# Kernel optimization log

Measured on AMD Instinct MI355X. Metric: run time of the kernel, lower is better.

The kernel has to match this reference:

```python
import jax, jax.numpy as jnp
import numpy as np

B = 16384   # batch of nodes
K = 15      # num_sample neighbors (default in forward)
U = 19997   # unique neighbor ids (prime so stride trick gives distinct ids)
D = 256     # feature dim


def setup_inputs() -> dict:
    key = jax.random.key(0)
    k1, k2, k3 = jax.random.split(key, 3)
    # Distinct-by-construction neighbor ids per row, mirroring random.sample
    # (set sampling => 15 distinct neighbors per node). start + step*(1..K) mod
    # prime U is injective in k for any step in [1, U-1].
    start = jax.random.randint(k1, (B, 1), 0, U)
    step = jax.random.randint(k2, (B, 1), 1, U)
    neigh_idx = ((start + step * jnp.arange(1, K + 1)[None, :]) % U).astype(jnp.int64)
    features = jax.random.normal(k3, (U, D), dtype=jnp.float32)
    return {"neigh_idx": neigh_idx, "features": features}


def reference(neigh_idx, features):
    # Original: one-hot mask [B, U], row-normalized by neighbor count, then
    # mask.mm(embed_matrix). With K distinct neighbors per row this is exactly
    # the mean of the gathered neighbor embeddings.
    gathered = features[neigh_idx]            # [B, K, D]
    return gathered.mean(axis=1)              # [B, D]
```

## Files before the change

kernel.cpp:

```cpp
#include <hip/hip_runtime.h>
#include <hip/hip_fp16.h>


#define K_NEIGH 15
#define D 256
#define ROW_U4 32

__global__ __launch_bounds__(256) void cvt_f32_to_f16(
    const float4* __restrict__ src,
    uint4* __restrict__ dst,
    int n8) {
  int i = blockIdx.x * 256 + threadIdx.x;
  if (i >= n8) return;
  float4 v0 = src[2 * i];
  float4 v1 = src[2 * i + 1];
  __half2 a = __floats2half2_rn(v0.x, v0.y);
  __half2 b = __floats2half2_rn(v0.z, v0.w);
  __half2 c = __floats2half2_rn(v1.x, v1.y);
  __half2 d = __floats2half2_rn(v1.z, v1.w);
  uint4 p;
  p.x = *reinterpret_cast<unsigned int*>(&a);
  p.y = *reinterpret_cast<unsigned int*>(&b);
  p.z = *reinterpret_cast<unsigned int*>(&c);
  p.w = *reinterpret_cast<unsigned int*>(&d);
  dst[i] = p;
}

__global__ __launch_bounds__(256) void MeanAggregator_46024869544579_kernel(
    const int* __restrict__ idx,
    const uint4* __restrict__ feat,
    float4* __restrict__ out,
    int B) {
  const int lane = threadIdx.x & 63;
  const int wave = blockIdx.x * 4 + (threadIdx.x >> 6);
  const int half = lane >> 5;
  const int sub = lane & 31;
  const int myrow = wave * 2 + half;
  if (myrow >= B) return;

  const int* rowidx = idx + (size_t)myrow * K_NEIGH;

  int j[K_NEIGH];
#pragma unroll
  for (int t = 0; t < K_NEIGH; ++t) j[t] = rowidx[t];

  uint4 v[K_NEIGH];
#pragma unroll
  for (int t = 0; t < K_NEIGH; ++t) {
    v[t] = feat[(size_t)j[t] * ROW_U4 + sub];
  }

  float acc[8];
#pragma unroll
  for (int i = 0; i < 8; ++i) acc[i] = 0.f;

#pragma unroll
  for (int t = 0; t < K_NEIGH; ++t) {
    const unsigned int* pv = &v[t].x;
#pragma unroll
    for (int q = 0; q < 4; ++q) {
      __half2 h = *reinterpret_cast<const __half2*>(&pv[q]);
      float2 f = __half22float2(h);
      acc[2 * q] += f.x;
      acc[2 * q + 1] += f.y;
    }
  }

  const float s = 1.0f / (float)K_NEIGH;
  float4 r0, r1;
  r0.x = acc[0] * s; r0.y = acc[1] * s; r0.z = acc[2] * s; r0.w = acc[3] * s;
  r1.x = acc[4] * s; r1.y = acc[5] * s; r1.z = acc[6] * s; r1.w = acc[7] * s;

  float4* orow = out + (size_t)myrow * (D / 4);
  orow[sub * 2] = r0;
  orow[sub * 2 + 1] = r1;
}

extern "C" void kernel_launch(void* const* d_in, const int* in_sizes, int n_in,
                              void* d_out, int out_size, void* d_ws, size_t ws_size,
                              hipStream_t stream) {
  const int* idx = (const int*)d_in[0];
  const float4* feat32 = (const float4*)d_in[1];
  float4* out = (float4*)d_out;

  const int B = in_sizes[0] / K_NEIGH;
  const int n8 = in_sizes[1] / 8;

  uint4* feat16 = (uint4*)d_ws;

  cvt_f32_to_f16<<<(n8 + 255) / 256, 256, 0, stream>>>(feat32, feat16, n8);

  const int grid = (B + 7) / 8;
  MeanAggregator_46024869544579_kernel<<<grid, 256, 0, stream>>>(idx, feat16, out, B);
}
```

Baseline: 90.16 us.

## Map one wavefront per row with lane-broadcast neighbor indices

Each wavefront now processes a single output row rather than two half-wave rows. Every lane loads an 8-byte fp16 chunk per neighbor instead of 16 bytes. The neighbor indices are loaded once per lane and broadcast with readlane, which makes them scalar and removes the redundant per-thread index loads. The grid doubles and launch bounds request higher occupancy, trading fewer bytes in flight per thread for more waves and cheaper address computation.

```diff
diff --git a/kernel.cpp b/kernel.cpp
--- a/kernel.cpp
+++ b/kernel.cpp
@@ -4,7 +4,7 @@
 
 #define K_NEIGH 15
 #define D 256
-#define ROW_U4 32
+#define ROW_U2 64
 
 __global__ __launch_bounds__(256) void cvt_f32_to_f16(
     const float4* __restrict__ src,
@@ -26,54 +26,40 @@
   dst[i] = p;
 }
 
-__global__ __launch_bounds__(256) void MeanAggregator_46024869544579_kernel(
+__global__ __launch_bounds__(256, 8) void MeanAggregator_46024869544579_kernel(
     const int* __restrict__ idx,
-    const uint4* __restrict__ feat,
+    const uint2* __restrict__ feat,
     float4* __restrict__ out,
     int B) {
   const int lane = threadIdx.x & 63;
   const int wave = blockIdx.x * 4 + (threadIdx.x >> 6);
-  const int half = lane >> 5;
-  const int sub = lane & 31;
-  const int myrow = wave * 2 + half;
-  if (myrow >= B) return;
+  if (wave >= B) return;
 
-  const int* rowidx = idx + (size_t)myrow * K_NEIGH;
+  const int* rowidx = idx + (size_t)wave * K_NEIGH;
+  int jl = rowidx[lane < K_NEIGH ? lane : 0];
 
-  int j[K_NEIGH];
-#pragma unroll
-  for (int t = 0; t < K_NEIGH; ++t) j[t] = rowidx[t];
-
-  uint4 v[K_NEIGH];
+  uint2 v[K_NEIGH];
 #pragma unroll
   for (int t = 0; t < K_NEIGH; ++t) {
-    v[t] = feat[(size_t)j[t] * ROW_U4 + sub];
+    int js = __builtin_amdgcn_readlane(jl, t);
+    v[t] = feat[(size_t)(unsigned)js * ROW_U2 + lane];
   }
 
-  float acc[8];
-#pragma unroll
-  for (int i = 0; i < 8; ++i) acc[i] = 0.f;
-
+  float a0 = 0.f, a1 = 0.f, a2 = 0.f, a3 = 0.f;
 #pragma unroll
   for (int t = 0; t < K_NEIGH; ++t) {
-    const unsigned int* pv = &v[t].x;
-#pragma unroll
-    for (int q = 0; q < 4; ++q) {
-      __half2 h = *reinterpret_cast<const __half2*>(&pv[q]);
-      float2 f = __half22float2(h);
-      acc[2 * q] += f.x;
-      acc[2 * q + 1] += f.y;
-    }
+    __half2 h0 = *reinterpret_cast<const __half2*>(&v[t].x);
+    __half2 h1 = *reinterpret_cast<const __half2*>(&v[t].y);
+    float2 f0 = __half22float2(h0);
+    float2 f1 = __half22float2(h1);
+    a0 += f0.x; a1 += f0.y; a2 += f1.x; a3 += f1.y;
   }
 
   const float s = 1.0f / (float)K_NEIGH;
-  float4 r0, r1;
-  r0.x = acc[0] * s; r0.y = acc[1] * s; r0.z = acc[2] * s; r0.w = acc[3] * s;
-  r1.x = acc[4] * s; r1.y = acc[5] * s; r1.z = acc[6] * s; r1.w = acc[7] * s;
+  float4 r;
+  r.x = a0 * s; r.y = a1 * s; r.z = a2 * s; r.w = a3 * s;
 
-  float4* orow = out + (size_t)myrow * (D / 4);
-  orow[sub * 2] = r0;
-  orow[sub * 2 + 1] = r1;
+  out[(size_t)wave * (D / 4) + lane] = r;
 }
 
 extern "C" void kernel_launch(void* const* d_in, const int* in_sizes, int n_in,
@@ -88,8 +74,9 @@
 
   uint4* feat16 = (uint4*)d_ws;
 
-  cvt_f32_to_f16<<<(n8 + 255) / 256, 256, 0, stream>>>(feat32, feat16, n8);
+  cvt_f32_to_f16<<<(n8 + 255) / 256, 256, 0, stream>>>(feat32, (uint4*)feat16, n8);
 
-  const int grid = (B + 7) / 8;
-  MeanAggregator_46024869544579_kernel<<<grid, 256, 0, stream>>>(idx, feat16, out, B);
+  const int grid = (B + 3) / 4;
+  MeanAggregator_46024869544579_kernel<<<grid, 256, 0, stream>>>(
+      idx, (const uint2*)feat16, out, B);
 }
```

Result: no change. 89.48 us (-0.8%).
